# Optimization experiments

Measured on AMD Instinct MI355X. Metric: run time of the kernel, lower is better.

## Reference

```python
import jax, jax.numpy as jnp
import numpy as np

DIM = 768
HEADS = 8

def setup_inputs() -> dict:
    key = jax.random.key(0)
    k1, k2, k3, k4 = jax.random.split(key, 4)
    x = jax.random.normal(k1, (4, 2048, DIM), dtype=jnp.float32)
    # torch Linear(D, 3D, bias=False): weight [3D, D]; store transposed [D, 3D]
    W_qkv = jax.random.normal(k2, (DIM, 3 * DIM), dtype=jnp.float32) * (DIM ** -0.5)
    W_o = jax.random.normal(k3, (DIM, DIM), dtype=jnp.float32) * (DIM ** -0.5)
    b_o = jax.random.normal(k4, (DIM,), dtype=jnp.float32) * 0.01
    return {"x": x, "W_qkv": W_qkv, "W_o": W_o, "b_o": b_o}

def reference(x, W_qkv, W_o, b_o):
    B, N, D = x.shape
    H = HEADS
    dh = D // H
    scale = dh ** -0.5
    qkv = x @ W_qkv                                   # [B, N, 3D]
    qkv = qkv.reshape(B, N, 3, H, dh)
    qkv = jnp.transpose(qkv, (2, 0, 3, 1, 4))         # [3, B, H, N, dh]
    Q, K, V = qkv[0], qkv[1], qkv[2]
    scores = jnp.einsum('bhqd,bhkd->bhqk', Q, K) * scale  # [B, H, N, N]
    attn = jax.nn.softmax(scores, axis=-1)
    out = jnp.einsum('bhqk,bhkd->bhqd', attn, V)      # [B, H, N, dh]
    # Faithful to original: reshape [B,H,N,dh] -> [B,N,D] WITHOUT head transpose
    out = out.reshape(B, N, D)
    return out @ W_o + b_o
```

## Files before the change

### kernel.cpp

```cpp
#include <hip/hip_runtime.h>

typedef __attribute__((ext_vector_type(8))) short short8;
typedef __attribute__((ext_vector_type(4))) float f32x4;
typedef __attribute__((ext_vector_type(4))) _Float16 half4;
typedef __attribute__((ext_vector_type(8))) _Float16 half8;
typedef __attribute__((ext_vector_type(2))) __fp16 fp16x2;

#define B_SZ 4
#define NSEQ 2048
#define DIM  768
#define NH   8
#define DH   96

__device__ __forceinline__ unsigned short f2bf(float f) {
  unsigned int u = __float_as_uint(f);
  u += 0x7fffu + ((u >> 16) & 1u);
  return (unsigned short)(u >> 16);
}

__device__ __forceinline__ float fexp2(float x) {
#if __has_builtin(__builtin_amdgcn_exp2f)
  return __builtin_amdgcn_exp2f(x);
#else
  return exp2f(x);
#endif
}

__device__ __forceinline__ void glds16(const void* g, void* l) {
  __builtin_amdgcn_global_load_lds((const __attribute__((address_space(1))) void*)g,
                                   (__attribute__((address_space(3))) void*)l, 16, 0, 0);
}

__global__ __launch_bounds__(256) void cvt_x_kernel(const float* __restrict__ x,
                                                    unsigned short* __restrict__ xb) {
  int i = blockIdx.x * 256 + threadIdx.x;
  float4 v = ((const float4*)x)[i];
  ushort4 o;
  o.x = f2bf(v.x); o.y = f2bf(v.y); o.z = f2bf(v.z); o.w = f2bf(v.w);
  ((ushort4*)xb)[i] = o;
}

__global__ __launch_bounds__(256) void transpose_cvt_kernel(const float* __restrict__ W,
                                                            unsigned short* __restrict__ WT,
                                                            int ncols) {
  __shared__ float tile[32][33];
  int tx = threadIdx.x, ty = threadIdx.y;
  int c0 = blockIdx.x * 32;
  int r0 = blockIdx.y * 32;
#pragma unroll
  for (int i = 0; i < 4; i++)
    tile[ty + i * 8][tx] = W[(size_t)(r0 + ty + i * 8) * ncols + c0 + tx];
  __syncthreads();
#pragma unroll
  for (int i = 0; i < 4; i++)
    WT[(size_t)(c0 + ty + i * 8) * 768 + r0 + tx] = f2bf(tile[tx][ty + i * 8]);
}

template <int EPI>
__global__ __launch_bounds__(256) void gemm_bt(
    const unsigned short* __restrict__ A, const unsigned short* __restrict__ Bt,
    unsigned short* __restrict__ qo, unsigned short* __restrict__ ko,
    _Float16* __restrict__ vo, float* __restrict__ fo,
    const float* __restrict__ bias)
{
  __shared__ unsigned short As[128 * 32];
  __shared__ unsigned short Bs[128 * 32];
  const int t = threadIdx.x;
  const int w = t >> 6, lane = t & 63;
  const int l15 = lane & 15, qd = lane >> 4;
  const int m0 = blockIdx.y * 128, n0 = blockIdx.x * 128;
  const int wm = (w >> 1) * 64, wn = (w & 1) * 64;

  const int sr = lane >> 2;
  const int sc = (lane & 3) * 8;
  const unsigned short* ga = A  + (size_t)(m0 + w * 16 + sr) * DIM + sc;
  const unsigned short* gb = Bt + (size_t)(n0 + w * 16 + sr) * DIM + sc;

  f32x4 acc[4][4] = {};

  for (int k0 = 0; k0 < DIM; k0 += 32) {
    glds16(ga + k0,            &As[w * 512]);
    glds16(ga + 64 * DIM + k0, &As[(4 + w) * 512]);
    glds16(gb + k0,            &Bs[w * 512]);
    glds16(gb + 64 * DIM + k0, &Bs[(4 + w) * 512]);
    __syncthreads();
    short8 af[4], bfr[4];
#pragma unroll
    for (int i = 0; i < 4; i++)
      af[i]  = *(const short8*)&As[(wm + i * 16 + l15) * 32 + qd * 8];
#pragma unroll
    for (int i = 0; i < 4; i++)
      bfr[i] = *(const short8*)&Bs[(wn + i * 16 + l15) * 32 + qd * 8];
#pragma unroll
    for (int mi = 0; mi < 4; mi++)
#pragma unroll
      for (int ni = 0; ni < 4; ni++)
        acc[mi][ni] = __builtin_amdgcn_mfma_f32_16x16x32_bf16(af[mi], bfr[ni], acc[mi][ni], 0, 0, 0);
    __syncthreads();
  }

#pragma unroll
  for (int mi = 0; mi < 4; mi++)
#pragma unroll
    for (int ni = 0; ni < 4; ni++) {
      int rowb = m0 + wm + mi * 16 + qd * 4;
      int col  = n0 + wn + ni * 16 + l15;
      if (EPI == 0) {
        int b = rowb >> 11, n = rowb & 2047;
        int s = col / DIM;
        int rem = col - s * DIM;
        int hh = rem / DH;
        int c = rem - hh * DH;
        size_t bh = (size_t)(b * NH + hh);
        if (s == 2) {
          half4 pk;
#pragma unroll
          for (int r = 0; r < 4; r++) pk[r] = (_Float16)acc[mi][ni][r];
          *(half4*)&vo[(bh * DH + c) * NSEQ + n] = pk;
        } else if (s == 0) {
#pragma unroll
          for (int r = 0; r < 4; r++)
            qo[(bh * NSEQ + n + r) * DH + c] = f2bf(acc[mi][ni][r] * 0.1472444679f);
        } else {
#pragma unroll
          for (int r = 0; r < 4; r++)
            ko[(bh * NSEQ + n + r) * DH + c] = f2bf(acc[mi][ni][r]);
        }
      } else {
#pragma unroll
        for (int r = 0; r < 4; r++)
          fo[(size_t)(rowb + r) * DIM + col] = acc[mi][ni][r] + bias[col];
      }
    }
}

__global__ __launch_bounds__(256, 4) void flash_kernel(
    const unsigned short* __restrict__ Qb, const unsigned short* __restrict__ Kb,
    const _Float16* __restrict__ Vtb, unsigned short* __restrict__ Z)
{
  __shared__ unsigned short Ks[64 * 96];
  __shared__ _Float16 Vs[96 * 64];

  const int t = threadIdx.x, w = t >> 6, lane = t & 63;
  const int l15 = lane & 15, qd = lane >> 4;
  const int swz = (l15 >> 1) & 3;
  const int vswz = l15 & 7;
  const int qt = blockIdx.x, h = blockIdx.y, b = blockIdx.z;
  const size_t bh = (size_t)(b * NH + h);
  const unsigned short* Qg = Qb + (bh * NSEQ + (size_t)qt * 64) * DH;
  const unsigned short* Kg = Kb + bh * NSEQ * DH;
  const _Float16*       Vg = Vtb + bh * (size_t)DH * NSEQ;

  int koff[3];
#pragma unroll
  for (int i = 0; i < 3; i++) {
    int L = w * 192 + i * 64 + lane;
    int r = L / 12, c = L - r * 12;
    int fk = r >> 4, m = r & 15;
    int key = 32 * (fk & 1) + 4 * (fk >> 1) + 8 * (m >> 2) + (m & 3);
    koff[i] = key * 96 + ((c ^ ((r >> 1) & 3)) * 8);
  }
  int voff[3];
#pragma unroll
  for (int i = 0; i < 3; i++) {
    int L = i * 256 + t;
    int r = L >> 3, c = L & 7;
    voff[i] = r * NSEQ + ((c ^ (r & 7)) * 8);
  }

#pragma unroll
  for (int i = 0; i < 3; i++)
    glds16(Qg + koff[i], &Ks[w * 1536 + i * 512]);
  __syncthreads();
  short8 qa[3];
#pragma unroll
  for (int ks = 0; ks < 3; ks++)
    qa[ks] = *(const short8*)&Ks[(w * 16 + l15) * 96 + ((ks * 4 + qd) ^ swz) * 8];

  f32x4 o[7] = {};
  float mprev = -1e30f;
  const half8 onef = {(_Float16)1.f, (_Float16)1.f, (_Float16)1.f, (_Float16)1.f,
                      (_Float16)1.f, (_Float16)1.f, (_Float16)1.f, (_Float16)1.f};

  for (int kt = 0; kt < 32; kt++) {
    __syncthreads();
    const unsigned short* Kt = Kg + (size_t)kt * 64 * DH;
#pragma unroll
    for (int i = 0; i < 3; i++)
      glds16(Kt + koff[i], &Ks[w * 1536 + i * 512]);
    const _Float16* Vt = Vg + kt * 64;
#pragma unroll
    for (int i = 0; i < 3; i++)
      glds16(Vt + voff[i], &Vs[(i * 256 + w * 64) * 8]);
    __syncthreads();

    f32x4 s[4] = {};
#pragma unroll
    for (int ks = 0; ks < 3; ks++)
#pragma unroll
      for (int fk = 0; fk < 4; fk++) {
        short8 kf = *(const short8*)&Ks[(fk * 16 + l15) * 96 + ((ks * 4 + qd) ^ swz) * 8];
        s[fk] = __builtin_amdgcn_mfma_f32_16x16x32_bf16(kf, qa[ks], s[fk], 0, 0, 0);
      }

    float mx = fmaxf(fmaxf(s[0][0], s[0][1]), fmaxf(s[0][2], s[0][3]));
#pragma unroll
    for (int fk = 1; fk < 4; fk++)
      mx = fmaxf(mx, fmaxf(fmaxf(s[fk][0], s[fk][1]), fmaxf(s[fk][2], s[fk][3])));
    mx = fmaxf(mx, __shfl_xor(mx, 16, 64));
    mx = fmaxf(mx, __shfl_xor(mx, 32, 64));
    float mnew = fmaxf(mprev, mx);
    float alpha = fexp2(mprev - mnew);
    mprev = mnew;

    half4 pf[4];
#pragma unroll
    for (int fk = 0; fk < 4; fk++) {
      union { fp16x2 h2[2]; half4 h4; } u;
      u.h2[0] = __builtin_amdgcn_cvt_pkrtz(fexp2(s[fk][0] - mnew), fexp2(s[fk][1] - mnew));
      u.h2[1] = __builtin_amdgcn_cvt_pkrtz(fexp2(s[fk][2] - mnew), fexp2(s[fk][3] - mnew));
      pf[fk] = u.h4;
    }
#pragma unroll
    for (int i = 0; i < 7; i++) o[i] = o[i] * alpha;

#pragma unroll
    for (int p = 0; p < 2; p++) {
      union { half4 h4[2]; half8 h8; } bu;
      bu.h4[0] = pf[p]; bu.h4[1] = pf[p + 2];
#pragma unroll
      for (int fc = 0; fc < 6; fc++) {
        half8 vf = *(const half8*)&Vs[(fc * 16 + l15) * 64 + ((p * 4 + qd) ^ vswz) * 8];
        o[fc] = __builtin_amdgcn_mfma_f32_16x16x32_f16(vf, bu.h8, o[fc], 0, 0, 0);
      }
      o[6] = __builtin_amdgcn_mfma_f32_16x16x32_f16(onef, bu.h8, o[6], 0, 0, 0);
    }
  }

  float inv = 1.0f / o[6][0];
  int qloc = 32 * (w & 1) + 4 * (w >> 1) + 8 * (l15 >> 2) + (l15 & 3);
  int q = qt * 64 + qloc;
  size_t zbase = ((size_t)b * NSEQ + h * 256 + (q >> 3)) * DIM + (q & 7) * DH;
#pragma unroll
  for (int fc = 0; fc < 6; fc++)
#pragma unroll
    for (int r = 0; r < 4; r += 2) {
      unsigned int pkd = (unsigned int)f2bf(o[fc][r] * inv)
                       | ((unsigned int)f2bf(o[fc][r + 1] * inv) << 16);
      *(unsigned int*)&Z[zbase + fc * 16 + qd * 4 + r] = pkd;
    }
}

extern "C" void kernel_launch(void* const* d_in, const int* in_sizes, int n_in,
                              void* d_out, int out_size, void* d_ws, size_t ws_size,
                              hipStream_t stream)
{
  (void)in_sizes; (void)n_in; (void)out_size; (void)ws_size;
  const float* x    = (const float*)d_in[0];
  const float* Wqkv = (const float*)d_in[1];
  const float* Wo   = (const float*)d_in[2];
  const float* bo   = (const float*)d_in[3];
  float* out = (float*)d_out;

  unsigned short* ws    = (unsigned short*)d_ws;
  unsigned short* xb    = ws;
  unsigned short* wqkvT = xb    + (size_t)8192 * 768;
  unsigned short* woT   = wqkvT + (size_t)2304 * 768;
  unsigned short* Qw    = woT   + (size_t)768 * 768;
  unsigned short* Kw    = Qw    + (size_t)6291456;
  _Float16*       Vw    = (_Float16*)(Kw + (size_t)6291456);
  unsigned short* Zw    = (unsigned short*)(Vw + (size_t)6291456);

  cvt_x_kernel<<<6144, 256, 0, stream>>>(x, xb);
  transpose_cvt_kernel<<<dim3(72, 24), dim3(32, 8), 0, stream>>>(Wqkv, wqkvT, 2304);
  transpose_cvt_kernel<<<dim3(24, 24), dim3(32, 8), 0, stream>>>(Wo, woT, 768);
  gemm_bt<0><<<dim3(18, 64), 256, 0, stream>>>(xb, wqkvT, Qw, Kw, Vw, nullptr, nullptr);
  flash_kernel<<<dim3(32, 8, 4), 256, 0, stream>>>(Qw, Kw, Vw, Zw);
  gemm_bt<1><<<dim3(6, 64), 256, 0, stream>>>(Zw, woT, nullptr, nullptr, nullptr, out, bo);
}
```

Before: 240.7 us.

## Fuse prep kernels, swizzle GEMM LDS, and widen flash blocks to 128 queries

The three conversion and transpose kernels are merged into one launch to cut launch overhead. The GEMM LDS tiles get an XOR swizzle to reduce bank conflicts on fragment reads. The flash attention block grows to 512 threads covering 128 queries, so each K/V tile load is shared by twice as many queries, with half the waves loading K and half loading V. The larger blocks can lower occupancy, and the grid drops to 512 blocks.

```diff
diff --git a/kernel.cpp b/kernel.cpp
--- a/kernel.cpp
+++ b/kernel.cpp
@@ -31,22 +31,26 @@
                                    (__attribute__((address_space(3))) void*)l, 16, 0, 0);
 }
 
-__global__ __launch_bounds__(256) void cvt_x_kernel(const float* __restrict__ x,
-                                                    unsigned short* __restrict__ xb) {
-  int i = blockIdx.x * 256 + threadIdx.x;
-  float4 v = ((const float4*)x)[i];
-  ushort4 o;
-  o.x = f2bf(v.x); o.y = f2bf(v.y); o.z = f2bf(v.z); o.w = f2bf(v.w);
-  ((ushort4*)xb)[i] = o;
-}
-
-__global__ __launch_bounds__(256) void transpose_cvt_kernel(const float* __restrict__ W,
-                                                            unsigned short* __restrict__ WT,
-                                                            int ncols) {
+__global__ __launch_bounds__(256) void prep_kernel(
+    const float* __restrict__ x, unsigned short* __restrict__ xb,
+    const float* __restrict__ Wqkv, unsigned short* __restrict__ wqkvT,
+    const float* __restrict__ Wo, unsigned short* __restrict__ woT)
+{
+  int blk = blockIdx.x;
+  if (blk < 6144) {
+    int i = blk * 256 + threadIdx.x;
+    float4 v = ((const float4*)x)[i];
+    ushort4 o;
+    o.x = f2bf(v.x); o.y = f2bf(v.y); o.z = f2bf(v.z); o.w = f2bf(v.w);
+    ((ushort4*)xb)[i] = o;
+    return;
+  }
   __shared__ float tile[32][33];
-  int tx = threadIdx.x, ty = threadIdx.y;
-  int c0 = blockIdx.x * 32;
-  int r0 = blockIdx.y * 32;
+  const float* W; unsigned short* WT; int ncols, bx, by;
+  if (blk < 7872) { int r = blk - 6144; W = Wqkv; WT = wqkvT; ncols = 2304; bx = r % 72; by = r / 72; }
+  else            { int r = blk - 7872; W = Wo;   WT = woT;   ncols = 768;  bx = r % 24; by = r / 24; }
+  int tx = threadIdx.x & 31, ty = threadIdx.x >> 5;
+  int c0 = bx * 32, r0 = by * 32;
 #pragma unroll
   for (int i = 0; i < 4; i++)
     tile[ty + i * 8][tx] = W[(size_t)(r0 + ty + i * 8) * ncols + c0 + tx];
@@ -68,11 +72,12 @@
   const int t = threadIdx.x;
   const int w = t >> 6, lane = t & 63;
   const int l15 = lane & 15, qd = lane >> 4;
+  const int asw = (l15 >> 1) & 3;
   const int m0 = blockIdx.y * 128, n0 = blockIdx.x * 128;
   const int wm = (w >> 1) * 64, wn = (w & 1) * 64;
 
   const int sr = lane >> 2;
-  const int sc = (lane & 3) * 8;
+  const int sc = ((lane & 3) ^ ((sr >> 1) & 3)) * 8;
   const unsigned short* ga = A  + (size_t)(m0 + w * 16 + sr) * DIM + sc;
   const unsigned short* gb = Bt + (size_t)(n0 + w * 16 + sr) * DIM + sc;
 
@@ -87,10 +92,10 @@
     short8 af[4], bfr[4];
 #pragma unroll
     for (int i = 0; i < 4; i++)
-      af[i]  = *(const short8*)&As[(wm + i * 16 + l15) * 32 + qd * 8];
+      af[i]  = *(const short8*)&As[(wm + i * 16 + l15) * 32 + (qd ^ asw) * 8];
 #pragma unroll
     for (int i = 0; i < 4; i++)
-      bfr[i] = *(const short8*)&Bs[(wn + i * 16 + l15) * 32 + qd * 8];
+      bfr[i] = *(const short8*)&Bs[(wn + i * 16 + l15) * 32 + (qd ^ asw) * 8];
 #pragma unroll
     for (int mi = 0; mi < 4; mi++)
 #pragma unroll
@@ -134,12 +139,14 @@
     }
 }
 
-__global__ __launch_bounds__(256, 4) void flash_kernel(
+__global__ __launch_bounds__(512, 4) void flash_kernel(
     const unsigned short* __restrict__ Qb, const unsigned short* __restrict__ Kb,
     const _Float16* __restrict__ Vtb, unsigned short* __restrict__ Z)
 {
-  __shared__ unsigned short Ks[64 * 96];
-  __shared__ _Float16 Vs[96 * 64];
+  __shared__ unsigned char smem[24576];
+  unsigned short* Qs = (unsigned short*)smem;
+  unsigned short* Ks = (unsigned short*)smem;
+  _Float16*       Vs = (_Float16*)(smem + 12288);
 
   const int t = threadIdx.x, w = t >> 6, lane = t & 63;
   const int l15 = lane & 15, qd = lane >> 4;
@@ -147,35 +154,44 @@
   const int vswz = l15 & 7;
   const int qt = blockIdx.x, h = blockIdx.y, b = blockIdx.z;
   const size_t bh = (size_t)(b * NH + h);
-  const unsigned short* Qg = Qb + (bh * NSEQ + (size_t)qt * 64) * DH;
+  const unsigned short* Qg = Qb + (bh * NSEQ + (size_t)qt * 128) * DH;
   const unsigned short* Kg = Kb + bh * NSEQ * DH;
   const _Float16*       Vg = Vtb + bh * (size_t)DH * NSEQ;
 
-  int koff[3];
+  int qoff[3];
 #pragma unroll
   for (int i = 0; i < 3; i++) {
-    int L = w * 192 + i * 64 + lane;
+    int L = i * 512 + t;
     int r = L / 12, c = L - r * 12;
-    int fk = r >> 4, m = r & 15;
-    int key = 32 * (fk & 1) + 4 * (fk >> 1) + 8 * (m >> 2) + (m & 3);
-    koff[i] = key * 96 + ((c ^ ((r >> 1) & 3)) * 8);
-  }
-  int voff[3];
-#pragma unroll
-  for (int i = 0; i < 3; i++) {
-    int L = i * 256 + t;
-    int r = L >> 3, c = L & 7;
-    voff[i] = r * NSEQ + ((c ^ (r & 7)) * 8);
+    qoff[i] = r * 96 + ((c ^ ((r >> 1) & 3)) * 8);
+  }
+  int soff[3];
+  if (w < 4) {
+#pragma unroll
+    for (int i = 0; i < 3; i++) {
+      int L = w * 192 + i * 64 + lane;
+      int r = L / 12, c = L - r * 12;
+      int fk = r >> 4, m = r & 15;
+      int key = 32 * (fk & 1) + 4 * (fk >> 1) + 8 * (m >> 2) + (m & 3);
+      soff[i] = key * 96 + ((c ^ ((r >> 1) & 3)) * 8);
+    }
+  } else {
+#pragma unroll
+    for (int i = 0; i < 3; i++) {
+      int L = i * 256 + (w - 4) * 64 + lane;
+      int r = L >> 3, c = L & 7;
+      soff[i] = r * NSEQ + ((c ^ (r & 7)) * 8);
+    }
   }
 
 #pragma unroll
   for (int i = 0; i < 3; i++)
-    glds16(Qg + koff[i], &Ks[w * 1536 + i * 512]);
+    glds16(Qg + qoff[i], &Qs[(i * 512 + w * 64) * 8]);
   __syncthreads();
   short8 qa[3];
 #pragma unroll
   for (int ks = 0; ks < 3; ks++)
-    qa[ks] = *(const short8*)&Ks[(w * 16 + l15) * 96 + ((ks * 4 + qd) ^ swz) * 8];
+    qa[ks] = *(const short8*)&Qs[(w * 16 + l15) * 96 + ((ks * 4 + qd) ^ swz) * 8];
 
   f32x4 o[7] = {};
   float mprev = -1e30f;
@@ -184,14 +200,17 @@
 
   for (int kt = 0; kt < 32; kt++) {
     __syncthreads();
-    const unsigned short* Kt = Kg + (size_t)kt * 64 * DH;
-#pragma unroll
-    for (int i = 0; i < 3; i++)
-      glds16(Kt + koff[i], &Ks[w * 1536 + i * 512]);
-    const _Float16* Vt = Vg + kt * 64;
-#pragma unroll
-    for (int i = 0; i < 3; i++)
-      glds16(Vt + voff[i], &Vs[(i * 256 + w * 64) * 8]);
+    if (w < 4) {
+      const unsigned short* Kt = Kg + (size_t)kt * 64 * DH;
+#pragma unroll
+      for (int i = 0; i < 3; i++)
+        glds16(Kt + soff[i], &Ks[w * 1536 + i * 512]);
+    } else {
+      const _Float16* Vt = Vg + kt * 64;
+#pragma unroll
+      for (int i = 0; i < 3; i++)
+        glds16(Vt + soff[i], &Vs[(i * 256 + (w - 4) * 64) * 8]);
+    }
     __syncthreads();
 
     f32x4 s[4] = {};
@@ -238,8 +257,7 @@
   }
 
   float inv = 1.0f / o[6][0];
-  int qloc = 32 * (w & 1) + 4 * (w >> 1) + 8 * (l15 >> 2) + (l15 & 3);
-  int q = qt * 64 + qloc;
+  int q = qt * 128 + w * 16 + l15;
   size_t zbase = ((size_t)b * NSEQ + h * 256 + (q >> 3)) * DIM + (q & 7) * DH;
 #pragma unroll
   for (int fc = 0; fc < 6; fc++)
@@ -271,10 +289,8 @@
   _Float16*       Vw    = (_Float16*)(Kw + (size_t)6291456);
   unsigned short* Zw    = (unsigned short*)(Vw + (size_t)6291456);
 
-  cvt_x_kernel<<<6144, 256, 0, stream>>>(x, xb);
-  transpose_cvt_kernel<<<dim3(72, 24), dim3(32, 8), 0, stream>>>(Wqkv, wqkvT, 2304);
-  transpose_cvt_kernel<<<dim3(24, 24), dim3(32, 8), 0, stream>>>(Wo, woT, 768);
+  prep_kernel<<<8448, 256, 0, stream>>>(x, xb, Wqkv, wqkvT, Wo, woT);
   gemm_bt<0><<<dim3(18, 64), 256, 0, stream>>>(xb, wqkvT, Qw, Kw, Vw, nullptr, nullptr);
-  flash_kernel<<<dim3(32, 8, 4), 256, 0, stream>>>(Qw, Kw, Vw, Zw);
+  flash_kernel<<<dim3(16, 8, 4), 512, 0, stream>>>(Qw, Kw, Vw, Zw);
   gemm_bt<1><<<dim3(6, 64), 256, 0, stream>>>(Zw, woT, nullptr, nullptr, nullptr, out, bo);
 }
```

Result: faster. 228.6 us (-5.0%).
